# Performance work log

Measured on AMD Instinct MI355X. Metric: run time of the kernel, lower is better.

The kernel has to match this reference:

```python
import jax, jax.numpy as jnp
import numpy as np

B, Q, K, D = 32, 2048, 2048, 128


def setup_inputs() -> dict:
    key = jax.random.key(0)
    kq, kk, kv, kl = jax.random.split(key, 4)
    q = jax.random.normal(kq, (B, Q, D), dtype=jnp.float32)
    k = jax.random.normal(kk, (B, K, D), dtype=jnp.float32)
    v = jax.random.normal(kv, (B, K, D), dtype=jnp.float32)
    # valid lengths in [1, K] so every row has at least one unmasked key
    valid_lens = jax.random.randint(kl, (B,), 1, K + 1, dtype=jnp.int32)
    return {"q": q, "k": k, "v": v, "valid_lens": valid_lens}


def reference(q, k, v, valid_lens):
    d = q.shape[-1]
    # [B, Q, K] scaled scores
    scores = jnp.einsum("bqd,bkd->bqk", q, k) / jnp.sqrt(jnp.asarray(d, q.dtype))
    # per-batch key mask: key index < valid_len  -> [B, 1, K]
    mask = jnp.arange(scores.shape[-1])[None, :] < valid_lens[:, None]  # [B, K]
    scores = jnp.where(mask[:, None, :], scores, -jnp.inf)
    attn = jax.nn.softmax(scores, axis=-1)  # dropout rate is 0.0 -> identity
    return jnp.einsum("bqk,bkd->bqd", attn, v)
```

## Files before the change

kernel.cpp:

```cpp
#include <hip/hip_runtime.h>


using bf16   = __bf16;
using bf16x4 = __attribute__((ext_vector_type(4)))  __bf16;
using bf16x8 = __attribute__((ext_vector_type(8)))  __bf16;
using f32x4  = __attribute__((ext_vector_type(4)))  float;
using f32x16 = __attribute__((ext_vector_type(16))) float;

constexpr int BATCH = 32;
constexpr int QLEN  = 2048;
constexpr int KLEN  = 2048;
constexpr int DH    = 128;
constexpr int QBLK  = 128;
constexpr int KVBLK = 64;
constexpr int NT    = KLEN / KVBLK;
constexpr int SPLIT_MIN_T = 14;

constexpr size_t OFF_KB    = 0;
constexpr size_t OFF_VB    = (size_t)16 << 20;
constexpr size_t OFF_HDR   = (size_t)32 << 20;
constexpr size_t OFF_ITEMS = OFF_HDR + 4096;
constexpr size_t OFF_L0    = OFF_HDR + 32768;
constexpr size_t OFF_L1    = OFF_L0 + ((size_t)256 << 10);
constexpr size_t OFF_PO    = OFF_L1 + ((size_t)256 << 10);
constexpr size_t PO_STRIDE = (size_t)1 << 20;

union U4f { bf16x4 h; uint2 u; };

__device__ __forceinline__ int swzK(int key, int byteoff) {
  return (key * 256 + byteoff) ^ ((key & 7) << 4);
}
__device__ __forceinline__ int swzV(int d, int byteoff) {
  return (d * 128 + byteoff) ^ (((d ^ (d >> 3)) & 7) << 4);
}

__device__ __forceinline__ void gld16(const void* g, void* l) {
  __builtin_amdgcn_global_load_lds(
      (const __attribute__((address_space(1))) void*)g,
      (__attribute__((address_space(3))) void*)l, 16, 0, 0);
}

__global__ __launch_bounds__(256)
void conv_kv(const float* __restrict__ Kg, const float* __restrict__ Vg,
             const int* __restrict__ Lg, bf16* __restrict__ KbT,
             bf16* __restrict__ VbT, int* __restrict__ hdr,
             int* __restrict__ items, int budget)
{
  __shared__ int sh_nt[32], sh_sp[32], sh_rk[32], sh_len[64];
  if (blockIdx.x == 0) {
    const int t = threadIdx.x;
    if (t < 32) {
      const int nt = (Lg[t] + KVBLK - 1) / KVBLK;
      int rank = 0;
      for (int j = 0; j < 32; ++j) {
        const int ntj = (Lg[j] + KVBLK - 1) / KVBLK;
        rank += (ntj > nt) || (ntj == nt && j < t);
      }
      const int sp = (nt >= SPLIT_MIN_T && rank < budget) ? 1 : 0;
      sh_nt[t] = nt; sh_sp[t] = sp; sh_rk[t] = rank;
      if (sp) hdr[8 + rank] = t;
    }
    __syncthreads();
    if (t < 64) {
      const int b = t >> 1, tl = t & 1;
      const int nt = sh_nt[b], sp = sh_sp[b];
      int tb, te;
      if (sp) { const int h = nt >> 1; tb = tl ? h : 0; te = tl ? nt : h; }
      else    { tb = 0; te = tl ? 0 : nt; }
      sh_len[t] = te - tb;
    }
    __syncthreads();
    if (t < 64) {
      const int len = sh_len[t];
      if (len > 0) {
        int r = 0;
        for (int j = 0; j < 64; ++j)
          r += (sh_len[j] > len) || (sh_len[j] == len && j < t);
        const int b = t >> 1, tl = t & 1;
        const int nt = sh_nt[b], sp = sh_sp[b];
        int tb = 0, te = nt;
        if (sp) { const int h = nt >> 1; tb = tl ? h : 0; te = tl ? nt : h; }
        const int slot = sp ? sh_rk[b] : 0;
        const int tailf = sp & tl;
        #pragma unroll
        for (int qq = 0; qq < 16; ++qq)
          items[r * 16 + qq] =
              b | (qq << 5) | (tb << 9) | (te << 15) | (sp << 21) |
              (tailf << 22) | (slot << 23);
      }
    }
    if (threadIdx.x == 0) {
      int ns = 0;
      for (int j = 0; j < 32; ++j) ns += sh_sp[j];
      hdr[0] = (32 + ns) * 16;
      hdr[1] = 0;
      hdr[2] = ns;
    }
  }

  constexpr int KCH = BATCH * NT * 64 * 16;
  constexpr int VCH = BATCH * NT * 8 * 128;
  const int stride = gridDim.x * blockDim.x;
  for (int i = blockIdx.x * blockDim.x + threadIdx.x; i < KCH + VCH; i += stride) {
    if (i < KCH) {
      const int i8  = i & 15;
      const int key = (i >> 4) & 63;
      const int kt  = (i >> 10) & 31;
      const int b   = i >> 15;
      const int Lb  = Lg[b];
      if (kt * 64 >= Lb) continue;
      const int k = kt * 64 + key;
      bf16x8 val = {};
      if (k < Lb) {
        const float* src = Kg + ((size_t)b * KLEN + k) * DH + i8 * 8;
        f32x4 a = *(const f32x4*)src;
        f32x4 c = *(const f32x4*)(src + 4);
        #pragma unroll
        for (int j = 0; j < 4; ++j) { val[j] = (bf16)a[j]; val[4 + j] = (bf16)c[j]; }
      }
      *(bf16x8*)((char*)KbT + (((size_t)b * NT + kt) << 14) + swzK(key, i8 * 16)) = val;
    } else {
      const int j2 = i - KCH;
      const int d  = j2 & 127;
      const int ko = (j2 >> 7) & 7;
      const int kt = (j2 >> 10) & 31;
      const int b  = j2 >> 15;
      const int Lb = Lg[b];
      if (kt * 64 >= Lb) continue;
      const int kb = kt * 64 + ko * 8;
      bf16x8 val = {};
      #pragma unroll
      for (int r = 0; r < 8; ++r) {
        float f = 0.f;
        if (kb + r < Lb) f = Vg[((size_t)b * KLEN + kb + r) * DH + d];
        val[r] = (bf16)f;
      }
      *(bf16x8*)((char*)VbT + (((size_t)b * NT + kt) << 14) + swzV(d, ko * 16)) = val;
    }
  }
}

__global__ __launch_bounds__(256, 2)
void fa_dyn(const float* __restrict__ Qg, const int* __restrict__ Lg,
            float* __restrict__ Og, const bf16* __restrict__ KbT,
            const bf16* __restrict__ VbT, const int* __restrict__ items,
            int* __restrict__ hdr, float* __restrict__ L0,
            float* __restrict__ L1, float* __restrict__ Po)
{
  __shared__ bf16 s_k [2][KVBLK * DH];
  __shared__ bf16 s_vt[2][KVBLK * DH];
  __shared__ int  s_item;

  const int tid  = threadIdx.x;
  const int wave = tid >> 6;
  const int lane = tid & 63;
  const int c    = lane & 31;
  const int hi   = lane >> 5;
  const float SC = 0.08838834764831845f * 1.4426950408889634f;

  const int n_items = hdr[0];

  for (;;) {
    if (tid == 0) s_item = atomicAdd(&hdr[1], 1);
    __syncthreads();
    const int it = s_item;
    if (it >= n_items) return;
    const int enc  = items[it];
    const int b    = enc & 31;
    const int qt   = (enc >> 5) & 15;
    const int tb   = (enc >> 9) & 63;
    const int te   = (enc >> 15) & 63;
    const int sp   = (enc >> 21) & 1;
    const int tail = (enc >> 22) & 1;
    const int slot = (enc >> 23) & 31;
    const int L    = Lg[b];

    const size_t baseQ = ((size_t)b * QLEN + (size_t)qt * QBLK) * DH;
    const char* Kbase = (const char*)KbT + (((size_t)b * NT) << 14);
    const char* Vbase = (const char*)VbT + (((size_t)b * NT) << 14);

    auto stageK = [&](int buf, int kt) {
      const char* tile = Kbase + ((size_t)kt << 14);
      #pragma unroll
      for (int s2 = 0; s2 < 4; ++s2) {
        const int off = wave * 4096 + s2 * 1024;
        gld16(tile + off + lane * 16, (char*)&s_k[buf][0] + off);
      }
    };
    auto stageV = [&](int buf, int kt) {
      const char* tile = Vbase + ((size_t)kt << 14);
      #pragma unroll
      for (int s2 = 0; s2 < 4; ++s2) {
        const int off = wave * 4096 + s2 * 1024;
        gld16(tile + off + lane * 16, (char*)&s_vt[buf][0] + off);
      }
    };

    bf16x8 qf[8];
    {
      const float* qp = Qg + baseQ + (size_t)(wave * 32 + c) * DH + hi * 8;
      #pragma unroll
      for (int dc = 0; dc < 8; ++dc) {
        f32x4 a = *(const f32x4*)(qp + dc * 16);
        f32x4 bb = *(const f32x4*)(qp + dc * 16 + 4);
        #pragma unroll
        for (int j = 0; j < 4; ++j) {
          qf[dc][j]     = (bf16)(a[j] * SC);
          qf[dc][4 + j] = (bf16)(bb[j] * SC);
        }
      }
    }

    f32x16 o[4];
    #pragma unroll
    for (int db = 0; db < 4; ++db)
      #pragma unroll
      for (int j = 0; j < 16; ++j) o[db][j] = 0.f;
    float l_acc = 0.f;

    stageK(0, tb);
    stageV(0, tb);
    __syncthreads();

    for (int kt = tb; kt < te; ++kt) {
      const int cur   = (kt - tb) & 1;
      const bool more = (kt + 1 < te);
      if (more) {
        stageK(cur ^ 1, kt + 1);
        stageV(cur ^ 1, kt + 1);
      }

      f32x16 st[2];
      __builtin_amdgcn_s_setprio(1);
      #pragma unroll
      for (int a = 0; a < 2; ++a) {
        #pragma unroll
        for (int j = 0; j < 16; ++j) st[a][j] = 0.f;
        const int key = a * 32 + c;
        #pragma unroll
        for (int dc = 0; dc < 8; ++dc) {
          bf16x8 kf = *(const bf16x8*)((const char*)&s_k[cur][0] +
                                       swzK(key, dc * 32 + hi * 16));
          st[a] = __builtin_amdgcn_mfma_f32_32x32x16_bf16(kf, qf[dc], st[a], 0, 0, 0);
        }
      }
      __builtin_amdgcn_s_setprio(0);

      const bool partial = ((kt + 1) * KVBLK > L);
      const int k0 = kt * KVBLK;
      #pragma unroll
      for (int a = 0; a < 2; ++a)
        #pragma unroll
        for (int r = 0; r < 16; ++r) {
          float p = __builtin_amdgcn_exp2f(st[a][r]);
          if (partial) {
            const int key = k0 + a * 32 + (r & 3) + 8 * (r >> 2) + 4 * hi;
            if (key >= L) p = 0.f;
          }
          st[a][r] = p;
          l_acc += p;
        }

      __builtin_amdgcn_s_setprio(1);
      #pragma unroll
      for (int kc = 0; kc < 4; ++kc) {
        const int a = kc >> 1, g = kc & 1;
        bf16x4 A, Bv;
        #pragma unroll
        for (int q2 = 0; q2 < 4; ++q2) {
          A[q2]  = (bf16)st[a][q2 + 8 * g];
          Bv[q2] = (bf16)st[a][q2 + 8 * g + 4];
        }
        U4f snd; snd.h = hi ? A : Bv;
        U4f rcv;
        rcv.u.x = (unsigned)__shfl_xor((int)snd.u.x, 32);
        rcv.u.y = (unsigned)__shfl_xor((int)snd.u.y, 32);
        bf16x4 loh = hi ? rcv.h : A;
        bf16x4 hih = hi ? Bv    : rcv.h;
        bf16x8 pa;
        #pragma unroll
        for (int q2 = 0; q2 < 4; ++q2) { pa[q2] = loh[q2]; pa[q2 + 4] = hih[q2]; }
        #pragma unroll
        for (int db = 0; db < 4; ++db) {
          const int d = db * 32 + c;
          bf16x8 vb = *(const bf16x8*)((const char*)&s_vt[cur][0] +
                                       swzV(d, kc * 32 + hi * 16));
          o[db] = __builtin_amdgcn_mfma_f32_32x32x16_bf16(pa, vb, o[db], 0, 0, 0);
        }
      }
      __builtin_amdgcn_s_setprio(0);

      if (more) __syncthreads();
    }

    const float l_row = l_acc + __shfl_xor(l_acc, 32);
    if (!sp) {
      float inv[16];
      #pragma unroll
      for (int j = 0; j < 16; ++j)
        inv[j] = 1.f / __shfl(l_row, (j & 3) + 8 * (j >> 2) + 4 * hi, 64);
      float* op = Og + baseQ + (size_t)(wave * 32) * DH;
      #pragma unroll
      for (int db = 0; db < 4; ++db)
        #pragma unroll
        for (int j = 0; j < 16; ++j) {
          const int row = (j & 3) + 8 * (j >> 2) + 4 * hi;
          op[(size_t)row * DH + db * 32 + c] = o[db][j] * inv[j];
        }
    } else {
      float* op = tail ? Po + ((size_t)(slot * 16 + qt) * 128 + wave * 32) * DH
                       : Og + baseQ + (size_t)(wave * 32) * DH;
      #pragma unroll
      for (int db = 0; db < 4; ++db)
        #pragma unroll
        for (int j = 0; j < 16; ++j) {
          const int row = (j & 3) + 8 * (j >> 2) + 4 * hi;
          op[(size_t)row * DH + db * 32 + c] = o[db][j];
        }
      float* Lp = (tail ? L1 : L0) + (slot * 16 + qt) * 128 + wave * 32;
      if (hi == 0) Lp[c] = l_row;
    }
  }
}

__global__ __launch_bounds__(256)
void combine(float* __restrict__ Og, const int* __restrict__ hdr,
             const float* __restrict__ L0, const float* __restrict__ L1,
             const float* __restrict__ Po)
{
  const int nsplit = hdr[2];
  const int total = nsplit << 16;
  for (int u = blockIdx.x * blockDim.x + threadIdx.x; u < total;
       u += gridDim.x * blockDim.x) {
    const int s   = u >> 16;
    const int q   = (u >> 12) & 15;
    const int row = (u >> 5) & 127;
    const int d4  = u & 31;
    const int b   = hdr[8 + s];
    const int li  = (s * 16 + q) * 128 + row;
    const float inv = 1.f / (L0[li] + L1[li]);
    const size_t og = ((size_t)b * QLEN + q * 128 + row) * DH + d4 * 4;
    const size_t po = ((size_t)(s * 16 + q) * 128 + row) * DH + d4 * 4;
    f32x4 a = *(const f32x4*)(Og + og);
    f32x4 p = *(const f32x4*)(Po + po);
    #pragma unroll
    for (int j = 0; j < 4; ++j) a[j] = (a[j] + p[j]) * inv;
    *(f32x4*)(Og + og) = a;
  }
}

__global__ __launch_bounds__(256)
void fa_fwd_sync(const float* __restrict__ Qg, const float* __restrict__ Kg,
                 const float* __restrict__ Vg, const int* __restrict__ Lg,
                 float* __restrict__ Og)
{
  __shared__ bf16 s_k[KVBLK * DH];
  __shared__ bf16 s_vt[DH * KVBLK];
  const int tid = threadIdx.x, wave = tid >> 6, lane = tid & 63;
  const int c = lane & 31, hi = lane >> 5;
  const int bid = blockIdx.x, batch = bid & 31, qtile = bid >> 5;
  const int L = Lg[batch], nt = (L + KVBLK - 1) / KVBLK;
  const size_t baseQ = ((size_t)batch * QLEN + (size_t)qtile * 128) * DH;
  const size_t baseKV = (size_t)batch * KLEN * DH;
  const float SC = 0.08838834764831845f * 1.4426950408889634f;
  bf16x8 qf[8];
  {
    const float* qp = Qg + baseQ + (size_t)(wave * 32 + c) * DH + hi * 8;
    #pragma unroll
    for (int dc = 0; dc < 8; ++dc) {
      f32x4 a = *(const f32x4*)(qp + dc * 16);
      f32x4 bb = *(const f32x4*)(qp + dc * 16 + 4);
      #pragma unroll
      for (int j = 0; j < 4; ++j) { qf[dc][j] = (bf16)(a[j]*SC); qf[dc][4+j] = (bf16)(bb[j]*SC); }
    }
  }
  f32x16 o[4];
  #pragma unroll
  for (int db = 0; db < 4; ++db)
    #pragma unroll
    for (int j = 0; j < 16; ++j) o[db][j] = 0.f;
  float l_acc = 0.f;
  for (int kt = 0; kt < nt; ++kt) {
    const int k0 = kt * KVBLK;
    __syncthreads();
    #pragma unroll
    for (int s = 0; s < 4; ++s) {
      const int id = tid + 256 * s, key = id >> 4, i8 = id & 15;
      bf16x8 val = {};
      if (k0 + key < L) {
        const float* src = Kg + baseKV + (size_t)(k0 + key) * DH + i8 * 8;
        f32x4 a = *(const f32x4*)src; f32x4 bb = *(const f32x4*)(src + 4);
        #pragma unroll
        for (int j = 0; j < 4; ++j) { val[j] = (bf16)a[j]; val[4+j] = (bf16)bb[j]; }
      }
      *(bf16x8*)((char*)s_k + swzK(key, i8 * 16)) = val;
    }
    {
      const int vp4 = tid >> 4, vi8 = tid & 15;
      bf16x8 rv[4];
      #pragma unroll
      for (int s = 0; s < 4; ++s) {
        bf16x8 val = {};
        if (k0 + 4 * vp4 + s < L) {
          const float* src = Vg + baseKV + (size_t)(k0 + 4 * vp4 + s) * DH + vi8 * 8;
          f32x4 a = *(const f32x4*)src; f32x4 bb = *(const f32x4*)(src + 4);
          #pragma unroll
          for (int j = 0; j < 4; ++j) { val[j] = (bf16)a[j]; val[4+j] = (bf16)bb[j]; }
        }
        rv[s] = val;
      }
      #pragma unroll
      for (int j = 0; j < 8; ++j) {
        bf16x4 w = { rv[0][j], rv[1][j], rv[2][j], rv[3][j] };
        *(bf16x4*)((char*)s_vt + swzV(vi8 * 8 + j, vp4 * 8)) = w;
      }
    }
    __syncthreads();
    f32x16 st[2];
    #pragma unroll
    for (int a = 0; a < 2; ++a) {
      #pragma unroll
      for (int j = 0; j < 16; ++j) st[a][j] = 0.f;
      const int key = a * 32 + c;
      #pragma unroll
      for (int dc = 0; dc < 8; ++dc) {
        bf16x8 kf = *(const bf16x8*)((const char*)s_k + swzK(key, dc * 32 + hi * 16));
        st[a] = __builtin_amdgcn_mfma_f32_32x32x16_bf16(kf, qf[dc], st[a], 0, 0, 0);
      }
    }
    const bool partial = (k0 + KVBLK > L);
    #pragma unroll
    for (int a = 0; a < 2; ++a)
      #pragma unroll
      for (int r = 0; r < 16; ++r) {
        float p = __builtin_amdgcn_exp2f(st[a][r]);
        if (partial) {
          const int key = k0 + a * 32 + (r & 3) + 8 * (r >> 2) + 4 * hi;
          if (key >= L) p = 0.f;
        }
        st[a][r] = p; l_acc += p;
      }
    #pragma unroll
    for (int kc = 0; kc < 4; ++kc) {
      const int a = kc >> 1, g = kc & 1;
      bf16x4 A, Bv;
      #pragma unroll
      for (int q2 = 0; q2 < 4; ++q2) { A[q2] = (bf16)st[a][q2+8*g]; Bv[q2] = (bf16)st[a][q2+8*g+4]; }
      U4f snd; snd.h = hi ? A : Bv;
      U4f rcv;
      rcv.u.x = (unsigned)__shfl_xor((int)snd.u.x, 32);
      rcv.u.y = (unsigned)__shfl_xor((int)snd.u.y, 32);
      bf16x4 loh = hi ? rcv.h : A;
      bf16x4 hih = hi ? Bv : rcv.h;
      bf16x8 pa;
      #pragma unroll
      for (int q2 = 0; q2 < 4; ++q2) { pa[q2] = loh[q2]; pa[q2+4] = hih[q2]; }
      #pragma unroll
      for (int db = 0; db < 4; ++db) {
        const int d = db * 32 + c;
        bf16x8 vb = *(const bf16x8*)((const char*)s_vt + swzV(d, kc * 32 + hi * 16));
        o[db] = __builtin_amdgcn_mfma_f32_32x32x16_bf16(pa, vb, o[db], 0, 0, 0);
      }
    }
  }
  const float l_row = l_acc + __shfl_xor(l_acc, 32);
  float inv[16];
  #pragma unroll
  for (int j = 0; j < 16; ++j)
    inv[j] = 1.f / __shfl(l_row, (j & 3) + 8 * (j >> 2) + 4 * hi, 64);
  float* op = Og + baseQ + (size_t)(wave * 32) * DH;
  #pragma unroll
  for (int db = 0; db < 4; ++db)
    #pragma unroll
    for (int j = 0; j < 16; ++j) {
      const int row = (j & 3) + 8 * (j >> 2) + 4 * hi;
      op[(size_t)row * DH + db * 32 + c] = o[db][j] * inv[j];
    }
}

extern "C" void kernel_launch(void* const* d_in, const int* in_sizes, int n_in,
                              void* d_out, int out_size, void* d_ws, size_t ws_size,
                              hipStream_t stream) {
  const float* q = (const float*)d_in[0];
  const float* k = (const float*)d_in[1];
  const float* v = (const float*)d_in[2];
  const int* lens = (const int*)d_in[3];
  float* out = (float*)d_out;

  if (ws_size >= OFF_L0) {
    char* W = (char*)d_ws;
    bf16* KbT = (bf16*)(W + OFF_KB);
    bf16* VbT = (bf16*)(W + OFF_VB);
    int*  hdr = (int*)(W + OFF_HDR);
    int*  items = (int*)(W + OFF_ITEMS);
    float* L0 = (float*)(W + OFF_L0);
    float* L1 = (float*)(W + OFF_L1);
    float* Po = (float*)(W + OFF_PO);
    int budget = 0;
    if (ws_size >= OFF_PO + PO_STRIDE)
      budget = (int)((ws_size - OFF_PO) / PO_STRIDE);
    if (budget > 32) budget = 32;
    hipLaunchKernelGGL(conv_kv, dim3(4096), dim3(256), 0, stream,
                       k, v, lens, KbT, VbT, hdr, items, budget);
    hipLaunchKernelGGL(fa_dyn, dim3(768), dim3(256), 0, stream,
                       q, lens, out, KbT, VbT, items, hdr, L0, L1, Po);
    hipLaunchKernelGGL(combine, dim3(1024), dim3(256), 0, stream,
                       out, hdr, L0, L1, Po);
  } else {
    hipLaunchKernelGGL(fa_fwd_sync, dim3(BATCH * (QLEN / QBLK)), dim3(256),
                       0, stream, q, k, v, lens, out);
  }
}
```

Before: 93.85 us.

## Load V tiles directly from global into registers instead of LDS staging

V is no longer staged through shared memory with async global-to-LDS copies. Each wave now reads its V fragments straight from global memory into registers (16 bf16x8 per lane) at the start of each KV tile. Only K stays double-buffered in LDS. This halves LDS usage, which may allow more occupancy, and removes LDS reads for V. In exchange the V loads are not prefetched a tile ahead, each wave fetches V redundantly from L2, and register pressure rises by 64 VGPRs, which may cause spills under launch_bounds(256,2).

```diff
diff --git a/kernel.cpp b/kernel.cpp
--- a/kernel.cpp
+++ b/kernel.cpp
@@ -147,8 +147,7 @@
             int* __restrict__ hdr, float* __restrict__ L0,
             float* __restrict__ L1, float* __restrict__ Po)
 {
-  __shared__ bf16 s_k [2][KVBLK * DH];
-  __shared__ bf16 s_vt[2][KVBLK * DH];
+  __shared__ bf16 s_k[2][KVBLK * DH];
   __shared__ int  s_item;
 
   const int tid  = threadIdx.x;
@@ -187,14 +186,6 @@
         gld16(tile + off + lane * 16, (char*)&s_k[buf][0] + off);
       }
     };
-    auto stageV = [&](int buf, int kt) {
-      const char* tile = Vbase + ((size_t)kt << 14);
-      #pragma unroll
-      for (int s2 = 0; s2 < 4; ++s2) {
-        const int off = wave * 4096 + s2 * 1024;
-        gld16(tile + off + lane * 16, (char*)&s_vt[buf][0] + off);
-      }
-    };
 
     bf16x8 qf[8];
     {
@@ -219,16 +210,21 @@
     float l_acc = 0.f;
 
     stageK(0, tb);
-    stageV(0, tb);
     __syncthreads();
 
     for (int kt = tb; kt < te; ++kt) {
       const int cur   = (kt - tb) & 1;
       const bool more = (kt + 1 < te);
-      if (more) {
-        stageK(cur ^ 1, kt + 1);
-        stageV(cur ^ 1, kt + 1);
-      }
+
+      const char* vtile = Vbase + ((size_t)kt << 14);
+      bf16x8 rV[4][4];
+      #pragma unroll
+      for (int kc = 0; kc < 4; ++kc)
+        #pragma unroll
+        for (int db = 0; db < 4; ++db)
+          rV[kc][db] = *(const bf16x8*)(vtile + swzV(db * 32 + c, kc * 32 + hi * 16));
+
+      if (more) stageK(cur ^ 1, kt + 1);
 
       f32x16 st[2];
       __builtin_amdgcn_s_setprio(1);
@@ -281,12 +277,8 @@
         #pragma unroll
         for (int q2 = 0; q2 < 4; ++q2) { pa[q2] = loh[q2]; pa[q2 + 4] = hih[q2]; }
         #pragma unroll
-        for (int db = 0; db < 4; ++db) {
-          const int d = db * 32 + c;
-          bf16x8 vb = *(const bf16x8*)((const char*)&s_vt[cur][0] +
-                                       swzV(d, kc * 32 + hi * 16));
-          o[db] = __builtin_amdgcn_mfma_f32_32x32x16_bf16(pa, vb, o[db], 0, 0, 0);
-        }
+        for (int db = 0; db < 4; ++db)
+          o[db] = __builtin_amdgcn_mfma_f32_32x32x16_bf16(pa, rV[kc][db], o[db], 0, 0, 0);
       }
       __builtin_amdgcn_s_setprio(0);
 
```

After: 110.9 us. 18.2% more time.
